# Optimization experiments

Hardware: AMD Instinct MI355X
Metric: run time of the kernel (lower is better)

## Reference

```python
import jax, jax.numpy as jnp
import numpy as np

NHEAD = 4
EPS_RMS = 1e-6
EPS_LN = 1e-5
KEEP_RATE = 0.7


def _adj_diag(num_joints=25):
    # NTU parent-child pairs; note torch.einsum('sjj,sntjc->sntjc', adj, x)
    # takes the DIAGONAL of each adjacency -> only adj_root (identity) survives,
    # adj_close/adj_far have zero diagonals. We reproduce that math faithfully.
    pairs = [(20, 1), (1, 0), (20, 2), (2, 3), (20, 4), (4, 5), (5, 6), (6, 7),
             (7, 21), (7, 22), (20, 8), (8, 9), (9, 10), (10, 11), (11, 23),
             (11, 24), (0, 12), (12, 13), (13, 14), (14, 15), (0, 16), (16, 17),
             (17, 18), (18, 19)]
    root = np.eye(num_joints, dtype=np.float32)
    close = np.zeros((num_joints, num_joints), dtype=np.float32)
    far = np.zeros((num_joints, num_joints), dtype=np.float32)
    for p, c in pairs:
        close[p, c] = 1.0
        far[c, p] = 1.0
    adj = np.stack([root, close, far])  # [3, J, J]
    return jnp.asarray(np.stack([np.diag(a) for a in adj]))  # [3, J]


def rmsnorm(x, w):
    return x * jax.lax.rsqrt(jnp.mean(x * x, -1, keepdims=True) + EPS_RMS) * w


def layernorm(x, w, b):
    m = jnp.mean(x, -1, keepdims=True)
    v = jnp.mean((x - m) ** 2, -1, keepdims=True)
    return (x - m) * jax.lax.rsqrt(v + EPS_LN) * w + b


def mha(x, in_w, in_b, out_w, out_b):
    # torch nn.MultiheadAttention (batch_first, eval: dropout off)
    B, L, C = x.shape
    H = NHEAD
    hd = C // H
    qkv = x @ in_w.T + in_b  # [B, L, 3C]
    q, k, v = jnp.split(qkv, 3, axis=-1)
    heads = lambda t: t.reshape(B, L, H, hd).transpose(0, 2, 1, 3)
    q, k, v = heads(q), heads(k), heads(v)
    attn = jax.nn.softmax(jnp.einsum('bhqd,bhkd->bhqk', q, k) / np.sqrt(hd).astype(np.float32), -1)
    o = jnp.einsum('bhqk,bhkd->bhqd', attn, v).transpose(0, 2, 1, 3).reshape(B, L, C)
    return o @ out_w.T + out_b, attn  # attn: [B, H, L, L] (average_attn_weights=False)


def reference(x, prev_spatial_attn_scores, gcn_w, g_norm_w, cls_tok, sn1_w, sn2_w,
              s_in_w, s_in_b, s_out_w, s_out_b, s_f1w, s_f1b, s_f2w, s_f2b,
              t_in_w, t_in_b, t_out_w, t_out_b, t_ln1w, t_ln1b, t_ln2w, t_ln2b,
              t_f1w, t_f1b, t_f2w, t_f2b, tn_w):
    N, T, J, _ = x.shape
    C = gcn_w.shape[-1]
    NT = N * T
    k = int(J * KEEP_RATE)
    diag = _adj_diag(J)  # [3, J]

    res = x  # residual = Identity (in_features == out_features)
    # ShiftGraphConvolution (diagonal einsum semantics) + RMSNorm
    x_gcn = rmsnorm(jnp.einsum('sj,ntjc,scd->ntjd', diag, x, gcn_w), g_norm_w)
    res_spatial = x_gcn
    xs = x_gcn.reshape(NT, J, C)

    # top-k token selection from previous cls-attention scores
    order = jnp.argsort(-prev_spatial_attn_scores, axis=1)  # descending
    idx_keep = order[:, :k]  # [NT, k]
    idx_drop = order[:, k:]  # [NT, J-k]
    ph_scores = jnp.take_along_axis(prev_spatial_attn_scores, idx_drop, 1)
    ph_norm = jax.nn.softmax(ph_scores, 1)[..., None]  # [NT, J-k, 1]
    x_inf = jnp.take_along_axis(xs, idx_keep[..., None], 1)  # [NT, k, C]
    x_ph = jnp.take_along_axis(xs, idx_drop[..., None], 1)   # [NT, J-k, C]
    x_rep = jnp.sum(x_ph * ph_norm, 1, keepdims=True)        # [NT, 1, C]

    cls = jnp.broadcast_to(cls_tok, (NT, 1, C))
    x_slow = jnp.concatenate([cls, x_inf, x_rep], 1)  # [NT, k+2, C]

    attn_out, attn_w = mha(rmsnorm(x_slow, sn1_w), s_in_w, s_in_b, s_out_w, s_out_b)
    x_msa = x_slow + attn_out
    ffn = jax.nn.gelu(rmsnorm(x_msa, sn2_w) @ s_f1w.T + s_f1b, approximate=False) @ s_f2w.T + s_f2b
    x_final_slow = x_msa + ffn

    # next spatial attention scores (cls -> other tokens, head-averaged)
    cls2others = attn_w[:, :, 0, 1:].mean(1)  # [NT, k+1]
    batch = jnp.arange(NT)[:, None]
    next_attn = jnp.zeros((NT, J), x.dtype)
    next_attn = next_attn.at[batch, idx_keep].set(cls2others[:, :k])
    next_attn = next_attn.at[batch, idx_drop].set(jnp.broadcast_to(cls2others[:, k:], (NT, J - k)))

    # scatter kept + placeholder tokens back to joint positions
    x_rep_res = attn_out[:, 1 + k:, :] + ffn[:, 1 + k:, :]  # [NT, 1, C]
    x_ph_out = x_ph + jnp.broadcast_to(x_rep_res, (NT, J - k, C))
    x_inf_out = x_final_slow[:, 1:1 + k, :]
    x_sp = jnp.zeros_like(xs)
    x_sp = x_sp.at[batch, idx_keep].set(x_inf_out)
    x_sp = x_sp.at[batch, idx_drop].set(x_ph_out)
    x_sp = x_sp.reshape(N, T, J, C) + res_spatial

    # temporal TransformerEncoderLayer (post-norm, gelu) + RMSNorm
    xt = x_sp.transpose(0, 2, 1, 3).reshape(N * J, T, C)
    a, _ = mha(xt, t_in_w, t_in_b, t_out_w, t_out_b)
    xt = layernorm(xt + a, t_ln1w, t_ln1b)
    f = jax.nn.gelu(xt @ t_f1w.T + t_f1b, approximate=False) @ t_f2w.T + t_f2b
    xt = layernorm(xt + f, t_ln2w, t_ln2b)
    xt = rmsnorm(xt, tn_w)
    x_t = xt.reshape(N, J, T, C).transpose(0, 2, 1, 3) + x_sp
    return x_t + res, next_attn


def setup_inputs() -> dict:
    key = jax.random.key(0)
    N, T, J, C, DFF = 64, 120, 25, 128, 256
    ks = jax.random.split(key, 16)
    g = lambda k_, shp: (jax.random.normal(k_, shp, jnp.float32) * 0.02)
    return {
        'x': jax.random.normal(ks[0], (N, T, J, C), jnp.float32),
        'prev_spatial_attn_scores': jax.random.uniform(ks[1], (N * T, J), jnp.float32),
        'gcn_w': g(ks[2], (3, C, C)),
        'g_norm_w': jnp.ones((C,), jnp.float32),
        'cls_tok': jnp.zeros((1, 1, C), jnp.float32),
        'sn1_w': jnp.ones((C,), jnp.float32),
        'sn2_w': jnp.ones((C,), jnp.float32),
        's_in_w': g(ks[3], (3 * C, C)), 's_in_b': jnp.zeros((3 * C,), jnp.float32),
        's_out_w': g(ks[4], (C, C)), 's_out_b': jnp.zeros((C,), jnp.float32),
        's_f1w': g(ks[5], (DFF, C)), 's_f1b': jnp.zeros((DFF,), jnp.float32),
        's_f2w': g(ks[6], (C, DFF)), 's_f2b': jnp.zeros((C,), jnp.float32),
        't_in_w': g(ks[7], (3 * C, C)), 't_in_b': jnp.zeros((3 * C,), jnp.float32),
        't_out_w': g(ks[8], (C, C)), 't_out_b': jnp.zeros((C,), jnp.float32),
        't_ln1w': jnp.ones((C,), jnp.float32), 't_ln1b': jnp.zeros((C,), jnp.float32),
        't_ln2w': jnp.ones((C,), jnp.float32), 't_ln2b': jnp.zeros((C,), jnp.float32),
        't_f1w': g(ks[9], (DFF, C)), 't_f1b': jnp.zeros((DFF,), jnp.float32),
        't_f2w': g(ks[10], (C, DFF)), 't_f2b': jnp.zeros((C,), jnp.float32),
        'tn_w': jnp.ones((C,), jnp.float32),
    }
```

## Files before the change

### kernel.cpp

```cpp
#include <hip/hip_runtime.h>
#include <hip/hip_bf16.h>
#include <math.h>

#define NTR   7680
#define NJ    25
#define NKEEP 17
#define NDRP  8
#define NL    19
#define NROW  192000
#define NTT   120
#define RSP   24

typedef __attribute__((ext_vector_type(8))) short bf16x8;
typedef __attribute__((ext_vector_type(4))) float f32x4;

__device__ __forceinline__ float gelu_exact(float v){
    return 0.5f * v * (1.0f + erff(v * 0.70710678118654752440f));
}
__device__ __forceinline__ unsigned short f2bf(float v){
    union { float f; unsigned u; } a; a.f = v;
    unsigned r = a.u + 0x7FFF + ((a.u >> 16) & 1);
    return (unsigned short)(r >> 16);
}
__device__ __forceinline__ float bf2f(unsigned short u){
    union { unsigned u; float f; } a; a.u = ((unsigned)u) << 16; return a.f;
}

__global__ void k_prep(const float* __restrict__ s_in_w, const float* __restrict__ s_out_w,
                       const float* __restrict__ s_f1w,  const float* __restrict__ s_f2w,
                       const float* __restrict__ t_in_w, const float* __restrict__ t_out_w,
                       const float* __restrict__ t_f1w,  const float* __restrict__ t_f2w,
                       const float* __restrict__ gcnw,   unsigned short* __restrict__ WM)
{
    int i = blockIdx.x * 256 + threadIdx.x;
    if (i < 65536){
        const float* src;
        int base;
        if      (i < 12288){ src = s_in_w;  base = 0; }
        else if (i < 16384){ src = s_out_w; base = 12288; }
        else if (i < 24576){ src = s_f1w;   base = 16384; }
        else if (i < 32768){ src = s_f2w;   base = 24576; }
        else if (i < 45056){ src = t_in_w;  base = 32768; }
        else if (i < 49152){ src = t_out_w; base = 45056; }
        else if (i < 57344){ src = t_f1w;   base = 49152; }
        else               { src = t_f2w;   base = 57344; }
        int loc = i - base;
        float4 v = *(const float4*)(src + loc * 4);
        ushort4 o; o.x = f2bf(v.x); o.y = f2bf(v.y); o.z = f2bf(v.z); o.w = f2bf(v.w);
        *(ushort4*)(WM + i * 4) = o;
    } else if (i < 81920){
        int j = i - 65536;
        int d = j >> 7, c = j & 127;
        WM[262144 + d * 128 + c] = f2bf(gcnw[c * 128 + d]);
    }
}

__global__ __launch_bounds__(256) void k_gcn_mfma(
    const float* __restrict__ x, const unsigned short* __restrict__ GWt,
    const float* __restrict__ gnw, unsigned short* __restrict__ xg)
{
    __shared__ __align__(16) unsigned short xb[64 * 136];
    __shared__ __align__(16) float yf[64 * 132];
    __shared__ float ssq[64];
    __shared__ float rstd[64];
    int tid = threadIdx.x, wv = tid >> 6, lane = tid & 63, cl = lane & 15, g = lane >> 4;
    size_t row0 = (size_t)blockIdx.x * 64;

    if (tid < 64) ssq[tid] = 0.f;
    const float4* x4 = (const float4*)(x + row0 * 128);
    for (int i = tid; i < 2048; i += 256){
        int row = i >> 5, ch = i & 31;
        float4 v = x4[row * 32 + ch];
        ushort4 o; o.x = f2bf(v.x); o.y = f2bf(v.y); o.z = f2bf(v.z); o.w = f2bf(v.w);
        *(ushort4*)(xb + row * 136 + ch * 4) = o;
    }
    __syncthreads();
    for (int job = wv; job < 32; job += 4){
        int rt = job >> 3, ct = job & 7, col = ct * 16 + cl;
        f32x4 acc = {0.f, 0.f, 0.f, 0.f};
        #pragma unroll
        for (int ks = 0; ks < 4; ks++){
            bf16x8 a = *(const bf16x8*)(xb + (rt*16 + cl)*136 + ks*32 + g*8);
            bf16x8 b = *(const bf16x8*)(GWt + col*128 + ks*32 + g*8);
            acc = __builtin_amdgcn_mfma_f32_16x16x32_bf16(a, b, acc, 0, 0, 0);
        }
        #pragma unroll
        for (int reg = 0; reg < 4; reg++){
            int row = rt*16 + g*4 + reg;
            float v = acc[reg];
            yf[row*132 + col] = v;
            float p = v * v;
            p += __shfl_xor(p, 1, 64); p += __shfl_xor(p, 2, 64);
            p += __shfl_xor(p, 4, 64); p += __shfl_xor(p, 8, 64);
            if (cl == 0) atomicAdd(&ssq[row], p);
        }
    }
    __syncthreads();
    if (tid < 64) rstd[tid] = rsqrtf(ssq[tid] * 0.0078125f + 1e-6f);
    __syncthreads();
    for (int i = tid; i < 2048; i += 256){
        int row = i >> 5, ch = i & 31;
        float4 v = *(const float4*)(yf + row*132 + ch*4);
        float4 w4 = *(const float4*)(gnw + ch*4);
        float r = rstd[row];
        ushort4 u;
        u.x = f2bf(v.x * r * w4.x); u.y = f2bf(v.y * r * w4.y);
        u.z = f2bf(v.z * r * w4.z); u.w = f2bf(v.w * r * w4.w);
        *(ushort4*)(xg + (row0 + row)*128 + ch*4) = u;
    }
}

__global__ void k_select(const float* __restrict__ sc, int* __restrict__ order,
                         int* __restrict__ slot, float* __restrict__ ph){
    int r = blockIdx.x * blockDim.x + threadIdx.x;
    if (r >= NTR) return;
    float s[NJ]; int id[NJ];
    for (int j = 0; j < NJ; j++){ s[j] = sc[r * NJ + j]; id[j] = j; }
    for (int m = 1; m < NJ; m++){
        float sv = s[m]; int iv = id[m]; int p = m;
        while (p > 0 && s[p-1] < sv){ s[p] = s[p-1]; id[p] = id[p-1]; p--; }
        s[p] = sv; id[p] = iv;
    }
    for (int j = 0; j < NJ; j++) order[r * NJ + j] = id[j];
    for (int i = 0; i < NKEEP; i++)  slot[r * NJ + id[i]] = 1 + i;
    for (int i = NKEEP; i < NJ; i++) slot[r * NJ + id[i]] = 18;
    float m8 = s[NKEEP];
    float e[NDRP]; float sum = 0.f;
    for (int i = 0; i < NDRP; i++){ e[i] = expf(s[NKEEP + i] - m8); sum += e[i]; }
    float inv = 1.f / sum;
    for (int i = 0; i < NDRP; i++) ph[r * NDRP + i] = e[i] * inv;
}

__global__ __launch_bounds__(512, 4) void k_spatial5(
    const unsigned short* __restrict__ xg, const int* __restrict__ order, const float* __restrict__ ph,
    const float* __restrict__ cls_tok, const float* __restrict__ sn1w, const float* __restrict__ sn2w,
    const unsigned short* __restrict__ WinB, const float* __restrict__ inb,
    const unsigned short* __restrict__ WoutB, const float* __restrict__ outb,
    const unsigned short* __restrict__ F1B, const float* __restrict__ f1b,
    const unsigned short* __restrict__ F2B, const float* __restrict__ f2b,
    unsigned short* __restrict__ delta, float* __restrict__ next_attn)
{
    __shared__ __align__(16) unsigned short sm[39680];
    __shared__ float rstd[48];
    __shared__ float ss2[48];
    __shared__ float clsp[8][20];
    __shared__ int   ord_s[2][NJ];
    __shared__ float ph_s[2][NDRP];
    unsigned short* xs = sm;
    unsigned short* xn = sm + 6528;
    unsigned short* Pb = sm + 6528;
    unsigned short* qk = sm + 16768;
    unsigned short* vT = sm + 29440;
    unsigned short* ao = sm + 29440;

    int tid = threadIdx.x;
    int r0 = blockIdx.x * 2;
    int wv = tid >> 6, lane = tid & 63, cl = lane & 15, g = lane >> 4;
    const float scale = 0.17677669529663687f;

    if (tid < 2*NJ)   ord_s[tid/NJ][tid%NJ] = order[(r0 + tid/NJ)*NJ + tid%NJ];
    if (tid < 2*NDRP) ph_s[tid>>3][tid&7]   = ph[(r0 + (tid>>3))*NDRP + (tid&7)];
    if (tid < 48) ss2[tid] = 0.f;
    for (int i = tid; i < 1280; i += 512)
        *(uint4*)(vT + i*8) = make_uint4(0,0,0,0);
    __syncthreads();

    {
        int ln = tid & 31;
        for (int j = tid >> 5; j < 48; j += 16){
            int rr = j / RSP, t = j - rr * RSP;
            const unsigned short* xgr = xg + (size_t)(r0 + rr) * NJ * 128;
            float v0, v1, v2, v3;
            if (t == 0){
                float4 cv = *(const float4*)(cls_tok + ln*4);
                v0 = cv.x; v1 = cv.y; v2 = cv.z; v3 = cv.w;
            } else if (t <= NKEEP){
                ushort4 u = *(const ushort4*)(xgr + ord_s[rr][t-1]*128 + ln*4);
                v0 = bf2f(u.x); v1 = bf2f(u.y); v2 = bf2f(u.z); v3 = bf2f(u.w);
            } else if (t == 18){
                v0 = v1 = v2 = v3 = 0.f;
                for (int i = 0; i < NDRP; i++){
                    ushort4 u = *(const ushort4*)(xgr + ord_s[rr][NKEEP+i]*128 + ln*4);
                    float w = ph_s[rr][i];
                    v0 = fmaf(bf2f(u.x),w,v0); v1 = fmaf(bf2f(u.y),w,v1);
                    v2 = fmaf(bf2f(u.z),w,v2); v3 = fmaf(bf2f(u.w),w,v3);
                }
            } else { v0 = v1 = v2 = v3 = 0.f; }
            ushort4 o4; o4.x=f2bf(v0); o4.y=f2bf(v1); o4.z=f2bf(v2); o4.w=f2bf(v3);
            *(ushort4*)(xs + j*136 + ln*4) = o4;
            float p = v0*v0 + v1*v1 + v2*v2 + v3*v3;
            p += __shfl_xor(p, 1, 64); p += __shfl_xor(p, 2, 64);
            p += __shfl_xor(p, 4, 64); p += __shfl_xor(p, 8, 64);
            p += __shfl_xor(p, 16, 64);
            if (ln == 0) rstd[j] = rsqrtf(p * 0.0078125f + 1e-6f);
        }
    }
    __syncthreads();

    {
        int c = tid & 127; float w = sn1w[c];
        for (int row = tid >> 7; row < 48; row += 4)
            xn[row*136 + c] = f2bf(bf2f(xs[row*136 + c]) * rstd[row] * w);
    }
    __syncthreads();

    {
        int col = wv*16 + cl;
        bf16x8 Bq[4], Bk[4], Bv[4];
        #pragma unroll
        for (int ks = 0; ks < 4; ks++){
            Bq[ks] = *(const bf16x8*)(WinB + col*128        + ks*32 + g*8);
            Bk[ks] = *(const bf16x8*)(WinB + (128+col)*128  + ks*32 + g*8);
            Bv[ks] = *(const bf16x8*)(WinB + (256+col)*128  + ks*32 + g*8);
        }
        float bq = inb[col], bk = inb[128+col], bv = inb[256+col];
        int h = col >> 5, d = col & 31;
        #pragma unroll
        for (int rt = 0; rt < 3; rt++){
            bf16x8 A[4];
            #pragma unroll
            for (int ks = 0; ks < 4; ks++)
                A[ks] = *(const bf16x8*)(xn + (rt*16 + cl)*136 + ks*32 + g*8);
            f32x4 aq = {0,0,0,0}, ak = {0,0,0,0}, av = {0,0,0,0};
            #pragma unroll
            for (int ks = 0; ks < 4; ks++){
                aq = __builtin_amdgcn_mfma_f32_16x16x32_bf16(A[ks], Bq[ks], aq, 0, 0, 0);
                ak = __builtin_amdgcn_mfma_f32_16x16x32_bf16(A[ks], Bk[ks], ak, 0, 0, 0);
                av = __builtin_amdgcn_mfma_f32_16x16x32_bf16(A[ks], Bv[ks], av, 0, 0, 0);
            }
            #pragma unroll
            for (int reg = 0; reg < 4; reg++){
                int row = rt*16 + g*4 + reg;
                qk[row*264 + col]       = f2bf((aq[reg] + bq) * scale);
                qk[row*264 + 128 + col] = f2bf(ak[reg] + bk);
                int rr = row >= RSP; int key = row - rr*RSP;
                vT[(rr*4 + h)*1280 + d*40 + key] = f2bf(av[reg] + bv);
            }
        }
    }
    __syncthreads();

    {
        int qh = wv;
        int rr = qh >> 2, h = qh & 3;
        bf16x8 aq[2];
        #pragma unroll
        for (int qt = 0; qt < 2; qt++)
            aq[qt] = *(const bf16x8*)(qk + (rr*RSP + qt*16 + cl)*264 + h*32 + g*8);
        f32x4 lg[2][2];
        #pragma unroll
        for (int kt = 0; kt < 2; kt++){
            bf16x8 bk = *(const bf16x8*)(qk + (rr*RSP + kt*16 + cl)*264 + 128 + h*32 + g*8);
            f32x4 z = {0.f, 0.f, 0.f, 0.f};
            lg[0][kt] = __builtin_amdgcn_mfma_f32_16x16x32_bf16(aq[0], bk, z, 0, 0, 0);
            lg[1][kt] = __builtin_amdgcn_mfma_f32_16x16x32_bf16(aq[1], bk, z, 0, 0, 0);
        }
        #pragma unroll
        for (int qt = 0; qt < 2; qt++){
            #pragma unroll
            for (int reg = 0; reg < 4; reg++){
                float l0 = lg[qt][0][reg];
                float l1 = (cl >= 3) ? -1e30f : lg[qt][1][reg];
                float m = fmaxf(l0, l1);
                m = fmaxf(m, __shfl_xor(m, 1, 64));
                m = fmaxf(m, __shfl_xor(m, 2, 64));
                m = fmaxf(m, __shfl_xor(m, 4, 64));
                m = fmaxf(m, __shfl_xor(m, 8, 64));
                float e0 = __expf(l0 - m), e1 = __expf(l1 - m);
                float ssum = e0 + e1;
                ssum += __shfl_xor(ssum, 1, 64); ssum += __shfl_xor(ssum, 2, 64);
                ssum += __shfl_xor(ssum, 4, 64); ssum += __shfl_xor(ssum, 8, 64);
                float inv = 1.f / ssum;
                e0 *= inv; e1 *= inv;
                int q = qt*16 + g*4 + reg;
                Pb[qh*1280 + q*40 + cl]      = f2bf(e0);
                Pb[qh*1280 + q*40 + 16 + cl] = f2bf(e1);
                if (qt == 0 && g == 0 && reg == 0){
                    clsp[qh][cl] = e0;
                    if (cl < 4) clsp[qh][16 + cl] = e1;
                }
            }
        }
        __syncthreads();
        bf16x8 ap[2];
        #pragma unroll
        for (int qt = 0; qt < 2; qt++)
            ap[qt] = *(const bf16x8*)(Pb + qh*1280 + (qt*16 + cl)*40 + g*8);
        #pragma unroll
        for (int dt = 0; dt < 2; dt++){
            bf16x8 bv = *(const bf16x8*)(vT + qh*1280 + (dt*16 + cl)*40 + g*8);
            #pragma unroll
            for (int qt = 0; qt < 2; qt++){
                f32x4 z = {0.f, 0.f, 0.f, 0.f};
                f32x4 oa = __builtin_amdgcn_mfma_f32_16x16x32_bf16(ap[qt], bv, z, 0, 0, 0);
                #pragma unroll
                for (int reg = 0; reg < 4; reg++){
                    int q = qt*16 + g*4 + reg;
                    if (q < 19)
                        qk[(rr*RSP + q)*264 + h*32 + dt*16 + cl] = f2bf(oa[reg]);
                    else if (q < RSP)
                        qk[(rr*RSP + q)*264 + h*32 + dt*16 + cl] = 0;
                }
            }
        }
        __syncthreads();
    }

    if (tid < 36){
        int rr2 = tid / 18, t = tid - rr2*18;
        float v = 0.25f * (clsp[rr2*4+0][1+t] + clsp[rr2*4+1][1+t] +
                           clsp[rr2*4+2][1+t] + clsp[rr2*4+3][1+t]);
        int r = r0 + rr2;
        if (t < NKEEP) next_attn[r*NJ + ord_s[rr2][t]] = v;
        else { for (int i = 0; i < NDRP; i++) next_attn[r*NJ + ord_s[rr2][NKEEP+i]] = v; }
    }

    {
        int col = wv*16 + cl;
        bf16x8 B[4];
        #pragma unroll
        for (int ks = 0; ks < 4; ks++)
            B[ks] = *(const bf16x8*)(WoutB + col*128 + ks*32 + g*8);
        float bias = outb[col];
        #pragma unroll
        for (int rt = 0; rt < 3; rt++){
            bf16x8 A[4];
            #pragma unroll
            for (int ks = 0; ks < 4; ks++)
                A[ks] = *(const bf16x8*)(qk + (rt*16 + cl)*264 + ks*32 + g*8);
            f32x4 acc = {0,0,0,0};
            #pragma unroll
            for (int ks = 0; ks < 4; ks++)
                acc = __builtin_amdgcn_mfma_f32_16x16x32_bf16(A[ks], B[ks], acc, 0, 0, 0);
            #pragma unroll
            for (int reg = 0; reg < 4; reg++){
                int row = rt*16 + g*4 + reg;
                float v = acc[reg] + bias;
                float msa = bf2f(xs[row*136 + col]) + v;
                ao[row*136 + col] = f2bf(v);
                xs[row*136 + col] = f2bf(msa);
                float p = msa * msa;
                p += __shfl_xor(p, 1, 64); p += __shfl_xor(p, 2, 64);
                p += __shfl_xor(p, 4, 64); p += __shfl_xor(p, 8, 64);
                if (cl == 0) atomicAdd(&ss2[row], p);
            }
        }
    }
    __syncthreads();

    if (tid < 48) rstd[tid] = rsqrtf(ss2[tid] * 0.0078125f + 1e-6f);
    __syncthreads();
    {
        int c = tid & 127; float w = sn2w[c];
        for (int row = tid >> 7; row < 48; row += 4)
            xn[row*136 + c] = f2bf(bf2f(xs[row*136 + c]) * rstd[row] * w);
    }
    __syncthreads();

    {
        int c0 = wv*16 + cl, c1 = c0 + 128;
        bf16x8 B0[4], B1[4];
        #pragma unroll
        for (int ks = 0; ks < 4; ks++){
            B0[ks] = *(const bf16x8*)(F1B + c0*128 + ks*32 + g*8);
            B1[ks] = *(const bf16x8*)(F1B + c1*128 + ks*32 + g*8);
        }
        float b0 = f1b[c0], b1 = f1b[c1];
        #pragma unroll
        for (int rt = 0; rt < 3; rt++){
            bf16x8 A[4];
            #pragma unroll
            for (int ks = 0; ks < 4; ks++)
                A[ks] = *(const bf16x8*)(xn + (rt*16 + cl)*136 + ks*32 + g*8);
            f32x4 a0 = {0,0,0,0}, a1 = {0,0,0,0};
            #pragma unroll
            for (int ks = 0; ks < 4; ks++){
                a0 = __builtin_amdgcn_mfma_f32_16x16x32_bf16(A[ks], B0[ks], a0, 0, 0, 0);
                a1 = __builtin_amdgcn_mfma_f32_16x16x32_bf16(A[ks], B1[ks], a1, 0, 0, 0);
            }
            #pragma unroll
            for (int reg = 0; reg < 4; reg++){
                int row = rt*16 + g*4 + reg;
                qk[row*264 + c0] = f2bf(gelu_exact(a0[reg] + b0));
                qk[row*264 + c1] = f2bf(gelu_exact(a1[reg] + b1));
            }
        }
    }
    __syncthreads();

    {
        int col = wv*16 + cl;
        bf16x8 B[8];
        #pragma unroll
        for (int ks = 0; ks < 8; ks++)
            B[ks] = *(const bf16x8*)(F2B + col*256 + ks*32 + g*8);
        float bias = f2b[col];
        #pragma unroll
        for (int rt = 0; rt < 3; rt++){
            bf16x8 A[8];
            #pragma unroll
            for (int ks = 0; ks < 8; ks++)
                A[ks] = *(const bf16x8*)(qk + (rt*16 + cl)*264 + ks*32 + g*8);
            f32x4 acc = {0,0,0,0};
            #pragma unroll
            for (int ks = 0; ks < 8; ks++)
                acc = __builtin_amdgcn_mfma_f32_16x16x32_bf16(A[ks], B[ks], acc, 0, 0, 0);
            #pragma unroll
            for (int reg = 0; reg < 4; reg++){
                int row = rt*16 + g*4 + reg;
                int rr = row >= RSP; int tok = row - rr*RSP;
                if (tok < 19){
                    float dv = acc[reg] + bias + bf2f(ao[row*136 + col]);
                    delta[((size_t)(r0 + rr)*19 + tok)*128 + col] = f2bf(dv);
                }
            }
        }
    }
}

__global__ void k_scatter3(const unsigned short* __restrict__ xg, const unsigned short* __restrict__ delta,
                           const int* __restrict__ slot, unsigned short* __restrict__ xb){
    int i = blockIdx.x * 256 + threadIdx.x;
    int e = i * 4;
    int c = e & 127; int rem = e >> 7;
    int t = rem % NTT; int nj = rem / NTT; int j = nj % NJ; int n = nj / NJ;
    int r = n * NTT + t;
    int sl = slot[r * NJ + j];
    ushort4 xv = *(const ushort4*)(xg + ((size_t)r * NJ + j) * 128 + c);
    ushort4 dv = *(const ushort4*)(delta + ((size_t)r * 19 + sl) * 128 + c);
    ushort4 ob;
    ob.x = f2bf(2.f * bf2f(xv.x) + bf2f(dv.x));
    ob.y = f2bf(2.f * bf2f(xv.y) + bf2f(dv.y));
    ob.z = f2bf(2.f * bf2f(xv.z) + bf2f(dv.z));
    ob.w = f2bf(2.f * bf2f(xv.w) + bf2f(dv.w));
    *(ushort4*)(xb + e) = ob;
}

__global__ __launch_bounds__(256) void k_tattn2(
    const unsigned short* __restrict__ xb, const unsigned short* __restrict__ Wb,
    const float* __restrict__ inb, unsigned short* __restrict__ o)
{
    __shared__ __align__(16) unsigned short smem[22656];
    unsigned short* q_s = smem;
    unsigned short* k_s = smem + 4800;
    unsigned short* vT  = smem + 9600;
    unsigned short* P_s = smem + 13952;

    int tid = threadIdx.x;
    int l = tid & 63, cl = l & 15, g = l >> 4, wv = tid >> 6;
    int nj = blockIdx.x >> 2;
    int h  = blockIdx.x & 3;

    vT[(tid >> 3) * 136 + 120 + (tid & 7)] = 0;

    const unsigned short* xrow = xb + (size_t)nj * (NTT * 128);
    const float scale = 0.17677669529663687f;

    bf16x8 bfr[6][4];
    float bias[6];
    #pragma unroll
    for (int pc = 0; pc < 6; ++pc){
        int p = pc >> 1, s = pc & 1;
        int col = p * 128 + h * 32 + s * 16 + cl;
        bias[pc] = inb[col];
        #pragma unroll
        for (int ks = 0; ks < 4; ++ks)
            bfr[pc][ks] = *(const bf16x8*)(Wb + col * 128 + ks * 32 + g * 8);
    }

    for (int mt = wv; mt < 8; mt += 4){
        bf16x8 af[4];
        #pragma unroll
        for (int ks = 0; ks < 4; ++ks)
            af[ks] = *(const bf16x8*)(xrow + (mt * 16 + cl) * 128 + ks * 32 + g * 8);
        #pragma unroll
        for (int pc = 0; pc < 6; ++pc){
            f32x4 acc = {0.f, 0.f, 0.f, 0.f};
            #pragma unroll
            for (int ks = 0; ks < 4; ++ks)
                acc = __builtin_amdgcn_mfma_f32_16x16x32_bf16(af[ks], bfr[pc][ks], acc, 0, 0, 0);
            int p = pc >> 1, s = pc & 1;
            int d = s * 16 + cl;
            #pragma unroll
            for (int reg = 0; reg < 4; ++reg){
                int t = mt * 16 + g * 4 + reg;
                if (t < NTT){
                    float v = acc[reg] + bias[pc];
                    if (p == 0)      q_s[t * 40 + d] = f2bf(v * scale);
                    else if (p == 1) k_s[t * 40 + d] = f2bf(v);
                    else             vT[d * 136 + t] = f2bf(v);
                }
            }
        }
    }
    __syncthreads();

    for (int s = 0; s < 2; ++s){
        int mt = wv + s * 4;
        bf16x8 aq = *(const bf16x8*)(q_s + (mt * 16 + cl) * 40 + g * 8);
        f32x4 lg[8];
        #pragma unroll
        for (int jt = 0; jt < 8; ++jt){
            bf16x8 bk = *(const bf16x8*)(k_s + (jt * 16 + cl) * 40 + g * 8);
            f32x4 z = {0.f, 0.f, 0.f, 0.f};
            lg[jt] = __builtin_amdgcn_mfma_f32_16x16x32_bf16(aq, bk, z, 0, 0, 0);
        }
        if (cl >= 8){ lg[7][0] = -1e30f; lg[7][1] = -1e30f; lg[7][2] = -1e30f; lg[7][3] = -1e30f; }

        float inv[4];
        #pragma unroll
        for (int reg = 0; reg < 4; ++reg){
            float m = lg[0][reg];
            #pragma unroll
            for (int jt = 1; jt < 8; ++jt) m = fmaxf(m, lg[jt][reg]);
            m = fmaxf(m, __shfl_xor(m, 1, 64));
            m = fmaxf(m, __shfl_xor(m, 2, 64));
            m = fmaxf(m, __shfl_xor(m, 4, 64));
            m = fmaxf(m, __shfl_xor(m, 8, 64));
            float sum = 0.f;
            #pragma unroll
            for (int jt = 0; jt < 8; ++jt){ float e = __expf(lg[jt][reg] - m); lg[jt][reg] = e; sum += e; }
            sum += __shfl_xor(sum, 1, 64); sum += __shfl_xor(sum, 2, 64);
            sum += __shfl_xor(sum, 4, 64); sum += __shfl_xor(sum, 8, 64);
            inv[reg] = 1.f / sum;
        }

        unsigned short* Pw = P_s + wv * 2176;
        #pragma unroll
        for (int jt = 0; jt < 8; ++jt){
            #pragma unroll
            for (int reg = 0; reg < 4; ++reg)
                Pw[(g * 4 + reg) * 136 + jt * 16 + cl] = f2bf(lg[jt][reg] * inv[reg]);
        }
        __syncthreads();

        bf16x8 ap[4];
        #pragma unroll
        for (int ks = 0; ks < 4; ++ks)
            ap[ks] = *(const bf16x8*)(Pw + cl * 136 + ks * 32 + g * 8);
        #pragma unroll
        for (int nt = 0; nt < 2; ++nt){
            f32x4 oacc = {0.f, 0.f, 0.f, 0.f};
            #pragma unroll
            for (int ks = 0; ks < 4; ++ks){
                bf16x8 bv = *(const bf16x8*)(vT + (nt * 16 + cl) * 136 + ks * 32 + g * 8);
                oacc = __builtin_amdgcn_mfma_f32_16x16x32_bf16(ap[ks], bv, oacc, 0, 0, 0);
            }
            #pragma unroll
            for (int reg = 0; reg < 4; ++reg){
                int t = mt * 16 + g * 4 + reg;
                if (t < NTT)
                    o[((size_t)nj * NTT + t) * 128 + h * 32 + nt * 16 + cl] = f2bf(oacc[reg]);
            }
        }
        __syncthreads();
    }
}

__global__ __launch_bounds__(256, 4) void k_tblock(
    const unsigned short* __restrict__ o, const unsigned short* __restrict__ WoB,
    const float* __restrict__ ob, const unsigned short* __restrict__ xbres,
    const float* __restrict__ lnw, const float* __restrict__ lnb,
    const unsigned short* __restrict__ F1B, const float* __restrict__ f1b,
    const unsigned short* __restrict__ F2B, const float* __restrict__ f2b,
    const float* __restrict__ ln2w, const float* __restrict__ ln2b,
    const float* __restrict__ tnw, const float* __restrict__ x,
    float* __restrict__ out)
{
    __shared__ __align__(16) float yf[32 * 132];
    __shared__ __align__(16) unsigned short xbuf[32 * 136];
    __shared__ int xib[32];
    int tid = threadIdx.x, wv = tid >> 6, lane = tid & 63, cl = lane & 15, g = lane >> 4;
    size_t row0 = (size_t)blockIdx.x * 32;

    if (tid < 32){
        int grow = (int)row0 + tid;
        int t = grow % NTT; int njq = grow / NTT; int j = njq % NJ; int n = njq / NJ;
        xib[tid] = ((n * NTT + t) * NJ + j) * 128;
    }

    {
        int c0 = wv*16 + cl, c1 = c0 + 64;
        bf16x8 B0[4], B1[4];
        #pragma unroll
        for (int ks = 0; ks < 4; ks++){
            B0[ks] = *(const bf16x8*)(WoB + c0*128 + ks*32 + g*8);
            B1[ks] = *(const bf16x8*)(WoB + c1*128 + ks*32 + g*8);
        }
        float b0 = ob[c0], b1 = ob[c1];
        #pragma unroll
        for (int rt = 0; rt < 2; rt++){
            bf16x8 A[4];
            #pragma unroll
            for (int ks = 0; ks < 4; ks++)
                A[ks] = *(const bf16x8*)(o + (row0 + rt*16 + cl)*128 + ks*32 + g*8);
            f32x4 a0 = {0,0,0,0}, a1 = {0,0,0,0};
            #pragma unroll
            for (int ks = 0; ks < 4; ks++){
                a0 = __builtin_amdgcn_mfma_f32_16x16x32_bf16(A[ks], B0[ks], a0, 0, 0, 0);
                a1 = __builtin_amdgcn_mfma_f32_16x16x32_bf16(A[ks], B1[ks], a1, 0, 0, 0);
            }
            #pragma unroll
            for (int reg = 0; reg < 4; reg++){
                int row = rt*16 + g*4 + reg;
                yf[row*132 + c0] = a0[reg] + b0 + bf2f(xbres[(row0 + row)*128 + c0]);
                yf[row*132 + c1] = a1[reg] + b1 + bf2f(xbres[(row0 + row)*128 + c1]);
            }
        }
    }
    __syncthreads();

    {
        int row = tid >> 3, sub = tid & 7;
        float4 v[4];
        float s1 = 0.f, s2 = 0.f;
        #pragma unroll
        for (int k = 0; k < 4; k++){
            v[k] = *(const float4*)(yf + row*132 + sub*16 + k*4);
            s1 += v[k].x + v[k].y + v[k].z + v[k].w;
            s2 += v[k].x*v[k].x + v[k].y*v[k].y + v[k].z*v[k].z + v[k].w*v[k].w;
        }
        s1 += __shfl_xor(s1, 1, 64); s2 += __shfl_xor(s2, 1, 64);
        s1 += __shfl_xor(s1, 2, 64); s2 += __shfl_xor(s2, 2, 64);
        s1 += __shfl_xor(s1, 4, 64); s2 += __shfl_xor(s2, 4, 64);
        float m = s1 * 0.0078125f;
        float rv = rsqrtf(s2 * 0.0078125f - m*m + 1e-5f);
        #pragma unroll
        for (int k = 0; k < 4; k++){
            float4 w4 = *(const float4*)(lnw + sub*16 + k*4);
            float4 b4 = *(const float4*)(lnb + sub*16 + k*4);
            ushort4 u;
            u.x = f2bf((v[k].x - m) * rv * w4.x + b4.x);
            u.y = f2bf((v[k].y - m) * rv * w4.y + b4.y);
            u.z = f2bf((v[k].z - m) * rv * w4.z + b4.z);
            u.w = f2bf((v[k].w - m) * rv * w4.w + b4.w);
            *(ushort4*)(xbuf + row*136 + sub*16 + k*4) = u;
        }
    }
    __syncthreads();

    unsigned short* hb = (unsigned short*)yf;
    #pragma unroll
    for (int s = 0; s < 4; s++){
        int c = wv*16 + cl + s*64;
        bf16x8 B[4];
        #pragma unroll
        for (int ks = 0; ks < 4; ks++)
            B[ks] = *(const bf16x8*)(F1B + c*128 + ks*32 + g*8);
        float bias = f1b[c];
        #pragma unroll
        for (int rt = 0; rt < 2; rt++){
            bf16x8 A[4];
            #pragma unroll
            for (int ks = 0; ks < 4; ks++)
                A[ks] = *(const bf16x8*)(xbuf + (rt*16 + cl)*136 + ks*32 + g*8);
            f32x4 acc = {0,0,0,0};
            #pragma unroll
            for (int ks = 0; ks < 4; ks++)
                acc = __builtin_amdgcn_mfma_f32_16x16x32_bf16(A[ks], B[ks], acc, 0, 0, 0);
            #pragma unroll
            for (int reg = 0; reg < 4; reg++){
                int row = rt*16 + g*4 + reg;
                hb[row*264 + c] = f2bf(gelu_exact(acc[reg] + bias));
            }
        }
    }
    __syncthreads();

    float ys[2][2][4];
    #pragma unroll
    for (int s = 0; s < 2; s++){
        int c = wv*16 + cl + s*64;
        bf16x8 B[8];
        #pragma unroll
        for (int ks = 0; ks < 8; ks++)
            B[ks] = *(const bf16x8*)(F2B + c*256 + ks*32 + g*8);
        float bias = f2b[c];
        #pragma unroll
        for (int rt = 0; rt < 2; rt++){
            bf16x8 A[8];
            #pragma unroll
            for (int ks = 0; ks < 8; ks++)
                A[ks] = *(const bf16x8*)(hb + (rt*16 + cl)*264 + ks*32 + g*8);
            f32x4 acc = {0,0,0,0};
            #pragma unroll
            for (int ks = 0; ks < 8; ks++)
                acc = __builtin_amdgcn_mfma_f32_16x16x32_bf16(A[ks], B[ks], acc, 0, 0, 0);
            #pragma unroll
            for (int reg = 0; reg < 4; reg++){
                int row = rt*16 + g*4 + reg;
                ys[s][rt][reg] = acc[reg] + bias + bf2f(xbuf[row*136 + c]);
            }
        }
    }
    __syncthreads();
    #pragma unroll
    for (int s = 0; s < 2; s++){
        int c = wv*16 + cl + s*64;
        #pragma unroll
        for (int rt = 0; rt < 2; rt++)
            #pragma unroll
            for (int reg = 0; reg < 4; reg++)
                yf[(rt*16 + g*4 + reg)*132 + c] = ys[s][rt][reg];
    }
    __syncthreads();

    {
        int row = tid >> 3, sub = tid & 7;
        float4 v[4];
        float s1 = 0.f, s2 = 0.f;
        #pragma unroll
        for (int k = 0; k < 4; k++){
            v[k] = *(const float4*)(yf + row*132 + sub*16 + k*4);
            s1 += v[k].x + v[k].y + v[k].z + v[k].w;
            s2 += v[k].x*v[k].x + v[k].y*v[k].y + v[k].z*v[k].z + v[k].w*v[k].w;
        }
        s1 += __shfl_xor(s1, 1, 64); s2 += __shfl_xor(s2, 1, 64);
        s1 += __shfl_xor(s1, 2, 64); s2 += __shfl_xor(s2, 2, 64);
        s1 += __shfl_xor(s1, 4, 64); s2 += __shfl_xor(s2, 4, 64);
        float m = s1 * 0.0078125f;
        float rv = rsqrtf(s2 * 0.0078125f - m*m + 1e-5f);
        float z[4][4];
        float s3 = 0.f;
        #pragma unroll
        for (int k = 0; k < 4; k++){
            float4 w4 = *(const float4*)(ln2w + sub*16 + k*4);
            float4 b4 = *(const float4*)(ln2b + sub*16 + k*4);
            z[k][0] = (v[k].x - m) * rv * w4.x + b4.x;
            z[k][1] = (v[k].y - m) * rv * w4.y + b4.y;
            z[k][2] = (v[k].z - m) * rv * w4.z + b4.z;
            z[k][3] = (v[k].w - m) * rv * w4.w + b4.w;
            s3 += z[k][0]*z[k][0] + z[k][1]*z[k][1] + z[k][2]*z[k][2] + z[k][3]*z[k][3];
        }
        s3 += __shfl_xor(s3, 1, 64); s3 += __shfl_xor(s3, 2, 64); s3 += __shfl_xor(s3, 4, 64);
        float sr = rsqrtf(s3 * 0.0078125f + 1e-6f);
        int xb0 = xib[row] + sub*16;
        #pragma unroll
        for (int k = 0; k < 4; k++){
            float4 tw4 = *(const float4*)(tnw + sub*16 + k*4);
            ushort4 xr = *(const ushort4*)(xbres + (row0 + row)*128 + sub*16 + k*4);
            float4 xv = *(const float4*)(x + xb0 + k*4);
            float4 ov;
            ov.x = z[k][0] * sr * tw4.x + bf2f(xr.x) + xv.x;
            ov.y = z[k][1] * sr * tw4.y + bf2f(xr.y) + xv.y;
            ov.z = z[k][2] * sr * tw4.z + bf2f(xr.z) + xv.z;
            ov.w = z[k][3] * sr * tw4.w + bf2f(xr.w) + xv.w;
            *(float4*)(out + xb0 + k*4) = ov;
        }
    }
}

extern "C" void kernel_launch(void* const* d_in, const int* in_sizes, int n_in,
                              void* d_out, int out_size, void* d_ws, size_t ws_size,
                              hipStream_t stream) {
    (void)in_sizes; (void)n_in; (void)out_size;
    const float* x      = (const float*)d_in[0];
    const float* sc     = (const float*)d_in[1];
    const float* gcnw   = (const float*)d_in[2];
    const float* gnw    = (const float*)d_in[3];
    const float* cls    = (const float*)d_in[4];
    const float* sn1    = (const float*)d_in[5];
    const float* sn2    = (const float*)d_in[6];
    const float* s_in_w = (const float*)d_in[7];
    const float* s_in_b = (const float*)d_in[8];
    const float* s_out_w= (const float*)d_in[9];
    const float* s_out_b= (const float*)d_in[10];
    const float* s_f1w  = (const float*)d_in[11];
    const float* s_f1b  = (const float*)d_in[12];
    const float* s_f2w  = (const float*)d_in[13];
    const float* s_f2b  = (const float*)d_in[14];
    const float* t_in_w = (const float*)d_in[15];
    const float* t_in_b = (const float*)d_in[16];
    const float* t_out_w= (const float*)d_in[17];
    const float* t_out_b= (const float*)d_in[18];
    const float* t_ln1w = (const float*)d_in[19];
    const float* t_ln1b = (const float*)d_in[20];
    const float* t_ln2w = (const float*)d_in[21];
    const float* t_ln2b = (const float*)d_in[22];
    const float* t_f1w  = (const float*)d_in[23];
    const float* t_f1b  = (const float*)d_in[24];
    const float* t_f2w  = (const float*)d_in[25];
    const float* t_f2b  = (const float*)d_in[26];
    const float* tnw    = (const float*)d_in[27];

    char* ws = (char*)d_ws;
    const size_t SZ_BIG = 98304000;
    char*  R1 = ws;
    char*  R2 = ws + SZ_BIG;
    char*  R3 = ws + 2 * SZ_BIG;
    char* p = ws + 3 * SZ_BIG;
    int*   ORD  = (int*)p;   p += 768000;
    int*   SLOT = (int*)p;   p += 768000;
    float* PH   = (float*)p; p += 245760;
    unsigned short* WM = (unsigned short*)p; p += 557056;
    if (ws_size < (size_t)(p - ws)) return;

    unsigned short* WinB  = WM;
    unsigned short* WoutB = WM + 49152;
    unsigned short* F1B   = WM + 65536;
    unsigned short* F2B   = WM + 98304;
    unsigned short* WB    = WM + 131072;
    unsigned short* WoBt  = WM + 180224;
    unsigned short* F1Bt  = WM + 196608;
    unsigned short* F2Bt  = WM + 229376;
    unsigned short* GWt   = WM + 262144;

    unsigned short* XG  = (unsigned short*)R1;
    unsigned short* DLT = (unsigned short*)R3;
    unsigned short* XB  = (unsigned short*)(R3 + 37355520);
    unsigned short* OB  = (unsigned short*)R2;

    float* out0 = (float*)d_out;
    float* next_attn = out0 + 24576000;

    k_prep<<<320, 256, 0, stream>>>(s_in_w, s_out_w, s_f1w, s_f2w,
                                    t_in_w, t_out_w, t_f1w, t_f2w, gcnw, WM);
    k_gcn_mfma<<<3000, 256, 0, stream>>>(x, GWt, gnw, XG);
    k_select<<<30, 256, 0, stream>>>(sc, ORD, SLOT, PH);
    k_spatial5<<<3840, 512, 0, stream>>>(XG, ORD, PH, cls, sn1, sn2,
                                         WinB, s_in_b, WoutB, s_out_b,
                                         F1B, s_f1b, F2B, s_f2b,
                                         DLT, next_attn);
    k_scatter3<<<24000, 256, 0, stream>>>(XG, DLT, SLOT, XB);
    k_tattn2<<<6400, 256, 0, stream>>>(XB, WB, t_in_b, OB);
    k_tblock<<<6000, 256, 0, stream>>>(OB, WoBt, t_out_b, XB,
                                       t_ln1w, t_ln1b, F1Bt, t_f1b,
                                       F2Bt, t_f2b, t_ln2w, t_ln2b,
                                       tnw, x, out0);
}
```

Measured before the change: 664.4 us.

## Fuse scatter residual into spatial kernel epilogue, drop delta buffer and slot map

The spatial attention kernel's final FFN epilogue now writes the residual result straight into the temporal-layout xb buffer. Kept tokens map through the per-row order, and the merged token's delta is broadcast to all eight dropped joints. This removes the separate scatter kernel, the intermediate delta round-trip through global memory and the slot array. In exchange the epilogue makes strided scalar bf16 stores and extra xg reads inside the spatial kernel, with a serial loop over dropped joints.

```diff
diff --git a/kernel.cpp b/kernel.cpp
--- a/kernel.cpp
+++ b/kernel.cpp
@@ -111,7 +111,7 @@
 }
 
 __global__ void k_select(const float* __restrict__ sc, int* __restrict__ order,
-                         int* __restrict__ slot, float* __restrict__ ph){
+                         float* __restrict__ ph){
     int r = blockIdx.x * blockDim.x + threadIdx.x;
     if (r >= NTR) return;
     float s[NJ]; int id[NJ];
@@ -122,8 +122,6 @@
         s[p] = sv; id[p] = iv;
     }
     for (int j = 0; j < NJ; j++) order[r * NJ + j] = id[j];
-    for (int i = 0; i < NKEEP; i++)  slot[r * NJ + id[i]] = 1 + i;
-    for (int i = NKEEP; i < NJ; i++) slot[r * NJ + id[i]] = 18;
     float m8 = s[NKEEP];
     float e[NDRP]; float sum = 0.f;
     for (int i = 0; i < NDRP; i++){ e[i] = expf(s[NKEEP + i] - m8); sum += e[i]; }
@@ -131,14 +129,14 @@
     for (int i = 0; i < NDRP; i++) ph[r * NDRP + i] = e[i] * inv;
 }
 
-__global__ __launch_bounds__(512, 4) void k_spatial5(
+__global__ __launch_bounds__(512, 4) void k_spatial6(
     const unsigned short* __restrict__ xg, const int* __restrict__ order, const float* __restrict__ ph,
     const float* __restrict__ cls_tok, const float* __restrict__ sn1w, const float* __restrict__ sn2w,
     const unsigned short* __restrict__ WinB, const float* __restrict__ inb,
     const unsigned short* __restrict__ WoutB, const float* __restrict__ outb,
     const unsigned short* __restrict__ F1B, const float* __restrict__ f1b,
     const unsigned short* __restrict__ F2B, const float* __restrict__ f2b,
-    unsigned short* __restrict__ delta, float* __restrict__ next_attn)
+    unsigned short* __restrict__ xb, float* __restrict__ next_attn)
 {
     __shared__ __align__(16) unsigned short sm[39680];
     __shared__ float rstd[48];
@@ -157,6 +155,14 @@
     int r0 = blockIdx.x * 2;
     int wv = tid >> 6, lane = tid & 63, cl = lane & 15, g = lane >> 4;
     const float scale = 0.17677669529663687f;
+
+    size_t xbase[2];
+    #pragma unroll
+    for (int rr = 0; rr < 2; rr++){
+        int r = r0 + rr;
+        int n = r / NTT, t = r - n * NTT;
+        xbase[rr] = ((size_t)n * 3000 + t) * 128;
+    }
 
     if (tid < 2*NJ)   ord_s[tid/NJ][tid%NJ] = order[(r0 + tid/NJ)*NJ + tid%NJ];
     if (tid < 2*NDRP) ph_s[tid>>3][tid&7]   = ph[(r0 + (tid>>3))*NDRP + (tid&7)];
@@ -409,31 +415,25 @@
             for (int reg = 0; reg < 4; reg++){
                 int row = rt*16 + g*4 + reg;
                 int rr = row >= RSP; int tok = row - rr*RSP;
-                if (tok < 19){
+                if (tok >= 1 && tok <= 18){
                     float dv = acc[reg] + bias + bf2f(ao[row*136 + col]);
-                    delta[((size_t)(r0 + rr)*19 + tok)*128 + col] = f2bf(dv);
+                    const unsigned short* xgr = xg + (size_t)(r0 + rr) * NJ * 128;
+                    if (tok <= NKEEP){
+                        int j = ord_s[rr][tok-1];
+                        xb[xbase[rr] + (size_t)j*15360 + col] =
+                            f2bf(2.f * bf2f(xgr[j*128 + col]) + dv);
+                    } else {
+                        #pragma unroll 1
+                        for (int i = 0; i < NDRP; i++){
+                            int j = ord_s[rr][NKEEP+i];
+                            xb[xbase[rr] + (size_t)j*15360 + col] =
+                                f2bf(2.f * bf2f(xgr[j*128 + col]) + dv);
+                        }
+                    }
                 }
             }
         }
     }
-}
-
-__global__ void k_scatter3(const unsigned short* __restrict__ xg, const unsigned short* __restrict__ delta,
-                           const int* __restrict__ slot, unsigned short* __restrict__ xb){
-    int i = blockIdx.x * 256 + threadIdx.x;
-    int e = i * 4;
-    int c = e & 127; int rem = e >> 7;
-    int t = rem % NTT; int nj = rem / NTT; int j = nj % NJ; int n = nj / NJ;
-    int r = n * NTT + t;
-    int sl = slot[r * NJ + j];
-    ushort4 xv = *(const ushort4*)(xg + ((size_t)r * NJ + j) * 128 + c);
-    ushort4 dv = *(const ushort4*)(delta + ((size_t)r * 19 + sl) * 128 + c);
-    ushort4 ob;
-    ob.x = f2bf(2.f * bf2f(xv.x) + bf2f(dv.x));
-    ob.y = f2bf(2.f * bf2f(xv.y) + bf2f(dv.y));
-    ob.z = f2bf(2.f * bf2f(xv.z) + bf2f(dv.z));
-    ob.w = f2bf(2.f * bf2f(xv.w) + bf2f(dv.w));
-    *(ushort4*)(xb + e) = ob;
 }
 
 __global__ __launch_bounds__(256) void k_tattn2(
@@ -790,7 +790,6 @@
     char*  R3 = ws + 2 * SZ_BIG;
     char* p = ws + 3 * SZ_BIG;
     int*   ORD  = (int*)p;   p += 768000;
-    int*   SLOT = (int*)p;   p += 768000;
     float* PH   = (float*)p; p += 245760;
     unsigned short* WM = (unsigned short*)p; p += 557056;
     if (ws_size < (size_t)(p - ws)) return;
@@ -806,8 +805,7 @@
     unsigned short* GWt   = WM + 262144;
 
     unsigned short* XG  = (unsigned short*)R1;
-    unsigned short* DLT = (unsigned short*)R3;
-    unsigned short* XB  = (unsigned short*)(R3 + 37355520);
+    unsigned short* XB  = (unsigned short*)R3;
     unsigned short* OB  = (unsigned short*)R2;
 
     float* out0 = (float*)d_out;
@@ -816,12 +814,11 @@
     k_prep<<<320, 256, 0, stream>>>(s_in_w, s_out_w, s_f1w, s_f2w,
                                     t_in_w, t_out_w, t_f1w, t_f2w, gcnw, WM);
     k_gcn_mfma<<<3000, 256, 0, stream>>>(x, GWt, gnw, XG);
-    k_select<<<30, 256, 0, stream>>>(sc, ORD, SLOT, PH);
-    k_spatial5<<<3840, 512, 0, stream>>>(XG, ORD, PH, cls, sn1, sn2,
+    k_select<<<30, 256, 0, stream>>>(sc, ORD, PH);
+    k_spatial6<<<3840, 512, 0, stream>>>(XG, ORD, PH, cls, sn1, sn2,
                                          WinB, s_in_b, WoutB, s_out_b,
                                          F1B, s_f1b, F2B, s_f2b,
-                                         DLT, next_attn);
-    k_scatter3<<<24000, 256, 0, stream>>>(XG, DLT, SLOT, XB);
+                                         XB, next_attn);
     k_tattn2<<<6400, 256, 0, stream>>>(XB, WB, t_in_b, OB);
     k_tblock<<<6000, 256, 0, stream>>>(OB, WoBt, t_out_b, XB,
                                        t_ln1w, t_ln1b, F1Bt, t_f1b,
```

Result: no change. 669.3 us (+0.7%).
